# Optimization experiments

Measured on AMD Instinct MI355X. Metric: run time of the kernel, lower is better.

## Reference

```python
import jax, jax.numpy as jnp
import numpy as np

PI = 3.141592653589793

# ---------------- smoothing-constant solvers (numpy, import time) -------------
# Quadratic smoothing b*(r-rc)^2 matched to value V and slope dV at r.
def _smooth(V, dV, r):
    rc = r - 2.0 * V / dV
    b = dV * dV / (4.0 * V)
    return float(b), float(rc)

def _f1c(a, r0, rc, rlow, rhigh):  # smoothed Morse (stacking / hbond radial)
    shift = (1.0 - np.exp(-a * (rc - r0))) ** 2
    def V(r):
        return (1.0 - np.exp(-a * (r - r0))) ** 2 - shift
    def dV(r):
        e = np.exp(-a * (r - r0))
        return 2.0 * (1.0 - e) * a * e
    blow, rclow = _smooth(V(rlow), dV(rlow), rlow)
    bhigh, rchigh = _smooth(V(rhigh), dV(rhigh), rhigh)
    return dict(a=a, r0=r0, shift=float(shift), rlow=rlow, rhigh=rhigh,
                blow=blow, rclow=rclow, bhigh=bhigh, rchigh=rchigh)

def _f2c(k, r0, rc, rlow, rhigh):  # smoothed harmonic well (cross/coaxial radial)
    dc2 = (rc - r0) ** 2
    def V(r):
        return 0.5 * k * ((r - r0) ** 2 - dc2)
    def dV(r):
        return k * (r - r0)
    blow, rclow = _smooth(V(rlow), dV(rlow), rlow)
    bhigh, rchigh = _smooth(V(rhigh), dV(rhigh), rhigh)
    return dict(k=k, r0=r0, dc2=float(dc2), rlow=rlow, rhigh=rhigh,
                blow=blow, rclow=rclow, bhigh=bhigh, rchigh=rchigh)

def _f3c(sigma, rstar):  # smoothed LJ excluded volume
    s6 = sigma ** 6
    V = 4.0 * (s6 * s6 / rstar ** 12 - s6 / rstar ** 6)
    dV = 4.0 * (-12.0 * s6 * s6 / rstar ** 13 + 6.0 * s6 / rstar ** 7)
    b, rc = _smooth(V, dV, rstar)
    return dict(sigma=sigma, rstar=rstar, b=b, rc=rc)

def _f4c(a, t0, ts):  # smoothed angular modulation 1-a*(th-t0)^2
    b = a * a * ts * ts / (1.0 - a * ts * ts)
    tc = ts + a * ts / b
    return dict(a=a, t0=t0, ts=ts, b=float(b), tc=float(tc))

def _f5c(a, xs):  # one-sided smoothed modulation on a cosine
    V = 1.0 - a * xs * xs
    dV = -2.0 * a * xs
    xc = xs - 2.0 * V / dV
    b = dV * dV / (4.0 * V)
    return dict(a=a, xs=xs, xc=float(xc), b=float(b))

FENE_EPS, FENE_R0, FENE_DELTA = 2.0, 0.7525, 0.25
F1_STCK = _f1c(6.0, 0.4, 0.9, 0.32, 0.75)
F1_HB = _f1c(8.0, 0.4, 0.75, 0.34, 0.70)
F2_CRST = _f2c(47.5, 0.575, 0.675, 0.495, 0.655)
F2_CX = _f2c(46.0, 0.4, 0.6, 0.22, 0.58)
F3_BACK = _f3c(0.70, 0.675)
F3_BASE = _f3c(0.33, 0.32)
F3_MIX = _f3c(0.515, 0.50)
F4 = dict(
    s4=_f4c(1.30, 0.0, 0.80), s5=_f4c(0.90, 0.0, 0.95), s6=_f4c(0.90, 0.0, 0.95),
    h1=_f4c(1.50, 0.0, 0.70), h2=_f4c(1.50, 0.0, 0.70), h3=_f4c(1.50, 0.0, 0.70),
    h4=_f4c(0.46, PI, 0.70), h7=_f4c(4.00, 0.5 * PI, 0.45), h8=_f4c(4.00, 0.5 * PI, 0.45),
    c1=_f4c(2.25, 0.791, 0.58), c2=_f4c(1.70, 1.003, 0.68), c3=_f4c(1.70, 1.003, 0.68),
    c4=_f4c(1.50, 0.0, 0.70), c7=_f4c(1.70, 0.555, 0.68), c8=_f4c(1.70, 0.555, 0.68),
    x1=_f4c(2.00, 2.592, 0.65), x4=_f4c(1.30, 0.0, 0.80))
F5C = _f5c(2.0, -0.65)
POS_BACK, POS_STACK, POS_BASE = -0.4, 0.34, 0.4

# ---------------- jnp piecewise potential pieces ------------------------------
def f1(r, c):
    e = jnp.exp(-c['a'] * (r - c['r0']))
    core = (1.0 - e) ** 2 - c['shift']
    v = jnp.where(r < c['rlow'], c['blow'] * (r - c['rclow']) ** 2,
        jnp.where(r < c['rhigh'], core, c['bhigh'] * (r - c['rchigh']) ** 2))
    return jnp.where((r > c['rclow']) & (r < c['rchigh']), v, 0.0)

def f2(r, c):
    core = 0.5 * c['k'] * ((r - c['r0']) ** 2 - c['dc2'])
    v = jnp.where(r < c['rlow'], c['blow'] * (r - c['rclow']) ** 2,
        jnp.where(r < c['rhigh'], core, c['bhigh'] * (r - c['rchigh']) ** 2))
    return jnp.where((r > c['rclow']) & (r < c['rchigh']), v, 0.0)

def f3(r, c, eps):
    x6 = (c['sigma'] / r) ** 6
    lj = 4.0 * (x6 * x6 - x6)
    v = jnp.where(r < c['rstar'], lj, c['b'] * (r - c['rc']) ** 2)
    return eps * jnp.where(r < c['rc'], v, 0.0)

def f4(theta, c):
    dt = jnp.abs(theta - c['t0'])
    v = jnp.where(dt < c['ts'], 1.0 - c['a'] * dt * dt, c['b'] * (c['tc'] - dt) ** 2)
    return jnp.where(dt < c['tc'], v, 0.0)

def f5(x, c):
    v = jnp.where(x > c['xs'], 1.0 - c['a'] * x * x, c['b'] * (c['xc'] - x) ** 2)
    v = jnp.where(x > 0.0, 1.0, v)
    return jnp.where(x > c['xc'], v, 0.0)

# ---------------- geometry helpers --------------------------------------------
def quat_axes(q):  # rotation-matrix rows a1,a2,a3, each (N,3)
    w, x, y, z = q[..., 0], q[..., 1], q[..., 2], q[..., 3]
    a1 = jnp.stack([w*w + x*x - y*y - z*z, 2*(x*y + w*z), 2*(x*z - w*y)], -1)
    a2 = jnp.stack([2*(x*y - w*z), w*w - x*x + y*y - z*z, 2*(y*z + w*x)], -1)
    a3 = jnp.stack([2*(x*z + w*y), 2*(y*z - w*x), w*w - x*x - y*y + z*z], -1)
    return a1, a2, a3

def min_image(d, box):
    return d - box * jnp.round(d / box)

def vnorm(d):
    return jnp.sqrt(jnp.sum(d * d, -1) + 1e-12)

def acos(c):
    return jnp.arccos(jnp.clip(c, -1.0 + 1e-6, 1.0 - 1e-6))

def dot(a, b):
    return jnp.sum(a * b, -1)

# ---------------- total oxDNA energy ------------------------------------------
def total_energy(positions, quaternions, box, stacking_eps, hbond_eps_matrix,
                 excl_eps, bonded_pairs, nonbonded_pairs, base_types):
    a1, a2, a3 = quat_axes(quaternions)
    back, stck, base = POS_BACK * a1, POS_STACK * a1, POS_BASE * a1
    bi, bj = bonded_pairs[:, 0], bonded_pairs[:, 1]
    ni, nj = nonbonded_pairs[:, 0], nonbonded_pairs[:, 1]

    def disp(si, sj, i, j):  # min-image site-to-site displacement, (P,3)
        return min_image((positions[j] + sj[j]) - (positions[i] + si[i]), box)

    # FENE (bonded backbone sites)
    rb = vnorm(disp(back, back, bi, bj))
    arg = jnp.clip(((rb - FENE_R0) / FENE_DELTA) ** 2, 0.0, 1.0 - 1e-6)
    e_fene = jnp.sum(-0.5 * FENE_EPS * jnp.log1p(-arg))

    # bonded excluded volume (base-base, back-base, base-back)
    e_bexc = jnp.sum(f3(vnorm(disp(base, base, bi, bj)), F3_BASE, excl_eps)
                     + f3(vnorm(disp(back, base, bi, bj)), F3_MIX, excl_eps)
                     + f3(vnorm(disp(base, back, bi, bj)), F3_MIX, excl_eps))

    # stacking (bonded stacking sites)
    ds = disp(stck, stck, bi, bj)
    rs = vnorm(ds)
    rhs = ds / rs[:, None]
    a3i, a3j, a2i, a2j = a3[bi], a3[bj], a2[bi], a2[bj]
    db = disp(back, back, bi, bj)
    rhb = db / vnorm(db)[:, None]
    th4, th5, th6 = acos(dot(a3i, a3j)), acos(dot(rhs, a3j)), acos(-dot(rhs, a3i))
    e_stck = jnp.sum(stacking_eps * f1(rs, F1_STCK)
                     * f4(th4, F4['s4']) * f4(th5, F4['s5']) * f4(th6, F4['s6'])
                     * f5(dot(a2i, rhb), F5C) * f5(dot(a2j, rhb), F5C))

    # nonbonded gathered frames
    A1i, A1j, A2i, A2j, A3i, A3j = a1[ni], a1[nj], a2[ni], a2[nj], a3[ni], a3[nj]

    # nonbonded excluded volume (all 4 site combos)
    e_nexc = jnp.sum(f3(vnorm(disp(back, back, ni, nj)), F3_BACK, excl_eps)
                     + f3(vnorm(disp(base, base, ni, nj)), F3_BASE, excl_eps)
                     + f3(vnorm(disp(back, base, ni, nj)), F3_MIX, excl_eps)
                     + f3(vnorm(disp(base, back, ni, nj)), F3_MIX, excl_eps))

    # hydrogen bonding (base sites)
    dh = disp(base, base, ni, nj)
    rh = vnorm(dh)
    rhh = dh / rh[:, None]
    t1, t2, t3 = acos(-dot(A1i, A1j)), acos(-dot(rhh, A1j)), acos(dot(rhh, A1i))
    t4, t7, t8 = acos(dot(A3i, A3j)), acos(-dot(rhh, A3j)), acos(dot(rhh, A3i))
    eps_hb = hbond_eps_matrix[base_types[ni], base_types[nj]]
    e_hb = jnp.sum(eps_hb * f1(rh, F1_HB)
                   * f4(t1, F4['h1']) * f4(t2, F4['h2']) * f4(t3, F4['h3'])
                   * f4(t4, F4['h4']) * f4(t7, F4['h7']) * f4(t8, F4['h8']))

    # cross stacking (base sites, same angles)
    e_cr = jnp.sum(f2(rh, F2_CRST)
                   * f4(t1, F4['c1']) * f4(t2, F4['c2']) * f4(t3, F4['c3'])
                   * f4(t4, F4['c4']) * f4(t7, F4['c7']) * f4(t8, F4['c8']))

    # coaxial stacking (stack sites)
    dx = disp(stck, stck, ni, nj)
    rx = vnorm(dx)
    rhx = dx / rx[:, None]
    e_cx = jnp.sum(f2(rx, F2_CX)
                   * f4(acos(-dot(A1i, A1j)), F4['x1']) * f4(acos(dot(A3i, A3j)), F4['x4'])
                   * f5(dot(A2i, rhx), F5C) * f5(dot(A2j, rhx), F5C))

    return e_fene + e_bexc + e_stck + e_nexc + e_hb + e_cr + e_cx


def setup_inputs() -> dict:
    N = 65536
    M = 16 * N
    k = jax.random.split(jax.random.key(0), 6)
    # random-walk chain: bonded neighbours land near the FENE minimum
    steps = jax.random.normal(k[0], (N, 3), dtype=jnp.float32)
    steps = 0.65 * steps / jnp.linalg.norm(steps, axis=-1, keepdims=True)
    positions = jnp.cumsum(steps, axis=0)
    q = jax.random.normal(k[1], (N, 4), dtype=jnp.float32)
    quaternions = q / jnp.linalg.norm(q, axis=-1, keepdims=True)
    box = jnp.full((3,), 200.0, dtype=jnp.float32)
    idx = jnp.arange(N - 1, dtype=jnp.int32)
    bonded_pairs = jnp.stack([idx, idx + 1], axis=1)
    i = jax.random.randint(k[2], (M,), 0, N - 8, dtype=jnp.int32)
    off = jax.random.randint(k[3], (M,), 2, 9, dtype=jnp.int32)
    nonbonded_pairs = jnp.stack([i, i + off], axis=1)  # near-in-chain => inside cutoffs
    base_types = jax.random.randint(k[4], (N,), 0, 4, dtype=jnp.int32)
    stacking_eps = 1.3 + 0.1 * jax.random.uniform(k[5], (N - 1,), dtype=jnp.float32)
    hb = np.zeros((4, 4), dtype=np.float32)  # A=0,C=1,G=2,T=3; only WC pairs bind
    hb[0, 3] = hb[3, 0] = hb[1, 2] = hb[2, 1] = 1.077
    return dict(positions=positions, quaternions=quaternions, box=box,
                stacking_eps=stacking_eps, hbond_eps_matrix=jnp.asarray(hb),
                excl_eps=jnp.float32(2.0), bonded_pairs=bonded_pairs,
                nonbonded_pairs=nonbonded_pairs, base_types=base_types)


def reference(positions, quaternions, box, stacking_eps, hbond_eps_matrix,
              excl_eps, bonded_pairs, nonbonded_pairs, base_types):
    return total_energy(positions, quaternions, box, stacking_eps,
                        hbond_eps_matrix, excl_eps,
                        bonded_pairs, nonbonded_pairs, base_types)
```

## Files before the change

kernel.cpp:

```cpp
#include <hip/hip_runtime.h>
#include <cmath>

#define DEV __device__ __forceinline__

struct F1C { float a, r0, shift, rlow, rhigh, blow, rclow, bhigh, rchigh; };
struct F2C { float k, r0, dc2, rlow, rhigh, blow, rclow, bhigh, rchigh; };
struct F3C { float sigma2, rstar, b, rc; };
struct F4C { float a, t0, ts, b, tc; };
struct F5P { float a, xs, xc, b; };

struct Params {
  F1C f1_stck, f1_hb;
  F2C f2_crst, f2_cx;
  F3C f3_back, f3_base, f3_mix;
  F4C s4, s5, h1, h4, h7, c1, c2, c7, x1;
  F5P f5;
};

struct V3 { float x, y, z; };
DEV V3 operator+(V3 a, V3 b) { return {a.x + b.x, a.y + b.y, a.z + b.z}; }
DEV V3 operator-(V3 a, V3 b) { return {a.x - b.x, a.y - b.y, a.z - b.z}; }
DEV V3 operator*(float s, V3 a) { return {s * a.x, s * a.y, s * a.z}; }
DEV float dot(V3 a, V3 b) { return a.x * b.x + a.y * b.y + a.z * b.z; }

DEV V3 mim(V3 d, V3 box, V3 ibox) {
  return { d.x - box.x * rintf(d.x * ibox.x),
           d.y - box.y * rintf(d.y * ibox.y),
           d.z - box.z * rintf(d.z * ibox.z) };
}

DEV void quat_axes(float4 q, V3& a1, V3& a2, V3& a3) {
  float w = q.x, x = q.y, y = q.z, z = q.w;
  float ww = w * w, xx = x * x, yy = y * y, zz = z * z;
  float xy = x * y, wz = w * z, xz = x * z, wy = w * y, yz = y * z, wx = w * x;
  a1 = { ww + xx - yy - zz, 2.f * (xy + wz), 2.f * (xz - wy) };
  a2 = { 2.f * (xy - wz), ww - xx + yy - zz, 2.f * (yz + wx) };
  a3 = { 2.f * (xz + wy), 2.f * (yz - wx), ww - xx - yy + zz };
}

DEV float acosc(float c) {
  c = fminf(fmaxf(c, -0.999999f), 0.999999f);
  return acosf(c);
}

DEV float f1f(float r, const F1C& c) {
  if (r <= c.rclow || r >= c.rchigh) return 0.f;
  if (r < c.rlow) { float d = r - c.rclow; return c.blow * d * d; }
  if (r < c.rhigh) {
    float ex = expf(-c.a * (r - c.r0));
    float t = 1.f - ex;
    return t * t - c.shift;
  }
  float d = r - c.rchigh; return c.bhigh * d * d;
}

DEV float f2f(float r, const F2C& c) {
  if (r <= c.rclow || r >= c.rchigh) return 0.f;
  if (r < c.rlow) { float d = r - c.rclow; return c.blow * d * d; }
  if (r < c.rhigh) { float d = r - c.r0; return 0.5f * c.k * (d * d - c.dc2); }
  float d = r - c.rchigh; return c.bhigh * d * d;
}

DEV float f3f(float r, float r2, const F3C& c, float eps) {
  if (r >= c.rc) return 0.f;
  float v;
  if (r < c.rstar) {
    float t = c.sigma2 / r2;
    float x6 = t * t * t;
    v = 4.f * (x6 * x6 - x6);
  } else {
    float d = r - c.rc; v = c.b * d * d;
  }
  return eps * v;
}

DEV float f4f(float th, const F4C& c) {
  float dt = fabsf(th - c.t0);
  if (dt >= c.tc) return 0.f;
  if (dt < c.ts) return 1.f - c.a * dt * dt;
  float d = c.tc - dt; return c.b * d * d;
}

DEV float f5f(float x, const F5P& c) {
  if (x <= c.xc) return 0.f;
  if (x > 0.f) return 1.f;
  if (x > c.xs) return 1.f - c.a * x * x;
  float d = c.xc - x; return c.b * d * d;
}

__global__ void __launch_bounds__(256)
energy_kernel(const float* __restrict__ pos,
              const float4* __restrict__ quat,
              const float* __restrict__ boxp,
              const float* __restrict__ seps,
              const float* __restrict__ hbm,
              const float* __restrict__ exclp,
              const int2* __restrict__ bp,
              const int2* __restrict__ nbp,
              const int* __restrict__ btype,
              int M, int NP, Params P,
              double* __restrict__ partials)
{
  int gid = blockIdx.x * 256 + threadIdx.x;
  float e = 0.f;
  if (gid < M + NP) {
    bool isNB = gid < M;
    int2 ij = isNB ? nbp[gid] : bp[gid - M];
    int i = ij.x, j = ij.y;

    const float* pi_ = pos + 3 * i;
    const float* pj_ = pos + 3 * j;
    V3 dp = { pj_[0] - pi_[0], pj_[1] - pi_[1], pj_[2] - pi_[2] };
    float4 qi = quat[i], qj = quat[j];
    V3 a1i, a2i, a3i, a1j, a2j, a3j;
    quat_axes(qi, a1i, a2i, a3i);
    quat_axes(qj, a1j, a2j, a3j);

    float bx = boxp[0], by = boxp[1], bz = boxp[2];
    V3 box = { bx, by, bz };
    V3 ibox = { 1.f / bx, 1.f / by, 1.f / bz };
    float excl = exclp[0];

    V3 s = a1j - a1i;
    V3 t = a1j + a1i;
    V3 dbb = mim(dp - 0.4f  * s, box, ibox);
    V3 dhh = mim(dp + 0.4f  * s, box, ibox);
    V3 dbB = mim(dp + 0.4f  * t, box, ibox);
    V3 dBb = mim(dp - 0.4f  * t, box, ibox);
    V3 dss = mim(dp + 0.34f * s, box, ibox);

    float rbb2 = dot(dbb, dbb) + 1e-12f; float rbb = sqrtf(rbb2);
    float rhh2 = dot(dhh, dhh) + 1e-12f; float rhh = sqrtf(rhh2);
    float rbB2 = dot(dbB, dbB) + 1e-12f; float rbB = sqrtf(rbB2);
    float rBb2 = dot(dBb, dBb) + 1e-12f; float rBb = sqrtf(rBb2);
    float rss2 = dot(dss, dss) + 1e-12f; float rss = sqrtf(rss2);

    e += f3f(rhh, rhh2, P.f3_base, excl);
    e += f3f(rbB, rbB2, P.f3_mix,  excl);
    e += f3f(rBb, rBb2, P.f3_mix,  excl);

    if (isNB) {
      e += f3f(rbb, rbb2, P.f3_back, excl);
      bool need1 = (rhh > P.f1_hb.rclow   && rhh < P.f1_hb.rchigh)
                || (rhh > P.f2_crst.rclow && rhh < P.f2_crst.rchigh);
      bool need2 = (rss > P.f2_cx.rclow   && rss < P.f2_cx.rchigh);
      if (need1 || need2) {
        float t1 = acosc(-dot(a1i, a1j));
        float t4 = acosc( dot(a3i, a3j));
        if (need1) {
          float ri = 1.f / rhh;
          V3 rh = ri * dhh;
          float t2 = acosc(-dot(rh, a1j));
          float t3 = acosc( dot(rh, a1i));
          float t7 = acosc(-dot(rh, a3j));
          float t8 = acosc( dot(rh, a3i));
          float f1v = f1f(rhh, P.f1_hb);
          if (f1v != 0.f) {
            float eps = hbm[btype[i] * 4 + btype[j]];
            if (eps != 0.f)
              e += eps * f1v * f4f(t1, P.h1) * f4f(t2, P.h1) * f4f(t3, P.h1)
                            * f4f(t4, P.h4) * f4f(t7, P.h7) * f4f(t8, P.h7);
          }
          float f2v = f2f(rhh, P.f2_crst);
          if (f2v != 0.f)
            e += f2v * f4f(t1, P.c1) * f4f(t2, P.c2) * f4f(t3, P.c2)
                     * f4f(t4, P.h1) * f4f(t7, P.c7) * f4f(t8, P.c7);
        }
        if (need2) {
          float f2x = f2f(rss, P.f2_cx);
          float ri = 1.f / rss;
          V3 rx = ri * dss;
          e += f2x * f4f(t1, P.x1) * f4f(t4, P.s4)
                   * f5f(dot(a2i, rx), P.f5) * f5f(dot(a2j, rx), P.f5);
        }
      }
    } else {
      float u = (rbb - 0.7525f) * 4.0f;
      float arg = fminf(u * u, 0.999999f);
      e += -log1pf(-arg);
      float f1v = f1f(rss, P.f1_stck);
      if (f1v != 0.f) {
        float ri = 1.f / rss;
        V3 rhs = ri * dss;
        float rbi = 1.f / rbb;
        V3 rhb = rbi * dbb;
        float th4 = acosc( dot(a3i, a3j));
        float th5 = acosc( dot(rhs, a3j));
        float th6 = acosc(-dot(rhs, a3i));
        e += seps[gid - M] * f1v * f4f(th4, P.s4) * f4f(th5, P.s5) * f4f(th6, P.s5)
                           * f5f(dot(a2i, rhb), P.f5) * f5f(dot(a2j, rhb), P.f5);
      }
    }
  }

  double v = (double)e;
  #pragma unroll
  for (int off = 32; off > 0; off >>= 1) v += __shfl_down(v, off, 64);
  __shared__ double sm[4];
  int lane = threadIdx.x & 63, wid = threadIdx.x >> 6;
  if (lane == 0) sm[wid] = v;
  __syncthreads();
  if (threadIdx.x == 0) partials[blockIdx.x] = sm[0] + sm[1] + sm[2] + sm[3];
}

__global__ void __launch_bounds__(1024)
finalize_kernel(const double* __restrict__ part, int n, float* __restrict__ out) {
  double v = 0.0;
  for (int i = threadIdx.x; i < n; i += 1024) v += part[i];
  #pragma unroll
  for (int off = 32; off > 0; off >>= 1) v += __shfl_down(v, off, 64);
  __shared__ double sm[16];
  int lane = threadIdx.x & 63, wid = threadIdx.x >> 6;
  if (lane == 0) sm[wid] = v;
  __syncthreads();
  if (wid == 0) {
    v = (lane < 16) ? sm[lane] : 0.0;
    #pragma unroll
    for (int off = 8; off > 0; off >>= 1) v += __shfl_down(v, off, 64);
    if (lane == 0) out[0] = (float)v;
  }
}

static inline double sqd(double x) { return x * x; }

static F1C mkf1(double a, double r0, double rc, double rlow, double rhigh) {
  double shift = sqd(1.0 - exp(-a * (rc - r0)));
  double el = exp(-a * (rlow - r0)), eh = exp(-a * (rhigh - r0));
  double Vl = sqd(1.0 - el) - shift, Vh = sqd(1.0 - eh) - shift;
  double dVl = 2.0 * (1.0 - el) * a * el, dVh = 2.0 * (1.0 - eh) * a * eh;
  double rclow = rlow - 2.0 * Vl / dVl, blow = dVl * dVl / (4.0 * Vl);
  double rchigh = rhigh - 2.0 * Vh / dVh, bhigh = dVh * dVh / (4.0 * Vh);
  return { (float)a, (float)r0, (float)shift, (float)rlow, (float)rhigh,
           (float)blow, (float)rclow, (float)bhigh, (float)rchigh };
}

static F2C mkf2(double k, double r0, double rc, double rlow, double rhigh) {
  double dc2 = sqd(rc - r0);
  double Vl = 0.5 * k * (sqd(rlow - r0) - dc2), Vh = 0.5 * k * (sqd(rhigh - r0) - dc2);
  double dVl = k * (rlow - r0), dVh = k * (rhigh - r0);
  double rclow = rlow - 2.0 * Vl / dVl, blow = dVl * dVl / (4.0 * Vl);
  double rchigh = rhigh - 2.0 * Vh / dVh, bhigh = dVh * dVh / (4.0 * Vh);
  return { (float)k, (float)r0, (float)dc2, (float)rlow, (float)rhigh,
           (float)blow, (float)rclow, (float)bhigh, (float)rchigh };
}

static F3C mkf3(double sigma, double rstar) {
  double s6 = pow(sigma, 6.0);
  double V = 4.0 * (s6 * s6 / pow(rstar, 12.0) - s6 / pow(rstar, 6.0));
  double dV = 4.0 * (-12.0 * s6 * s6 / pow(rstar, 13.0) + 6.0 * s6 / pow(rstar, 7.0));
  double rc = rstar - 2.0 * V / dV, b = dV * dV / (4.0 * V);
  return { (float)(sigma * sigma), (float)rstar, (float)b, (float)rc };
}

static F4C mkf4(double a, double t0, double ts) {
  double b = a * a * ts * ts / (1.0 - a * ts * ts);
  double tc = ts + a * ts / b;
  return { (float)a, (float)t0, (float)ts, (float)b, (float)tc };
}

static F5P mkf5(double a, double xs) {
  double V = 1.0 - a * xs * xs, dV = -2.0 * a * xs;
  double xc = xs - 2.0 * V / dV, b = dV * dV / (4.0 * V);
  return { (float)a, (float)xs, (float)xc, (float)b };
}

extern "C" void kernel_launch(void* const* d_in, const int* in_sizes, int n_in,
                              void* d_out, int out_size, void* d_ws, size_t ws_size,
                              hipStream_t stream) {
  (void)n_in; (void)out_size; (void)ws_size;
  const double PI = 3.141592653589793;

  const float*  pos  = (const float*)d_in[0];
  const float4* quat = (const float4*)d_in[1];
  const float*  box  = (const float*)d_in[2];
  const float*  seps = (const float*)d_in[3];
  const float*  hbm  = (const float*)d_in[4];
  const float*  excl = (const float*)d_in[5];
  const int2*   bp   = (const int2*)d_in[6];
  const int2*   nbp  = (const int2*)d_in[7];
  const int*    bt   = (const int*)d_in[8];

  int NP = in_sizes[6] / 2;
  int M  = in_sizes[7] / 2;
  int total = M + NP;
  int blocks = (total + 255) / 256;

  Params P;
  P.f1_stck = mkf1(6.0, 0.4, 0.9, 0.32, 0.75);
  P.f1_hb   = mkf1(8.0, 0.4, 0.75, 0.34, 0.7);
  P.f2_crst = mkf2(47.5, 0.575, 0.675, 0.495, 0.655);
  P.f2_cx   = mkf2(46.0, 0.4, 0.6, 0.22, 0.58);
  P.f3_back = mkf3(0.7, 0.675);
  P.f3_base = mkf3(0.33, 0.32);
  P.f3_mix  = mkf3(0.515, 0.5);
  P.s4 = mkf4(1.3, 0.0, 0.8);
  P.s5 = mkf4(0.9, 0.0, 0.95);
  P.h1 = mkf4(1.5, 0.0, 0.7);
  P.h4 = mkf4(0.46, PI, 0.7);
  P.h7 = mkf4(4.0, 0.5 * PI, 0.45);
  P.c1 = mkf4(2.25, 0.791, 0.58);
  P.c2 = mkf4(1.7, 1.003, 0.68);
  P.c7 = mkf4(1.7, 0.555, 0.68);
  P.x1 = mkf4(2.0, 2.592, 0.65);
  P.f5 = mkf5(2.0, -0.65);

  double* partials = (double*)d_ws;

  energy_kernel<<<blocks, 256, 0, stream>>>(pos, quat, box, seps, hbm, excl,
                                            bp, nbp, bt, M, NP, P, partials);
  finalize_kernel<<<1, 1024, 0, stream>>>(partials, blocks, (float*)d_out);
}
```

Before: 116.1 us.

## Compact nonbonded angular work into a separate kernel and use fast intrinsics

The main kernel now computes only the radial and excluded-volume terms. It uses a wave ballot with an atomic counter to compact the indices of nonbonded pairs that fall inside the hbond, cross-stacking or coaxial ranges. A second grid-stride kernel recomputes a reduced geometry for those pairs and evaluates the acos-heavy angular terms densely, so the divergent branch no longer stalls whole wavefronts. Division, sqrt and exp are also swapped for hardware rcp/sqrt/__expf intrinsics. The cost is two extra launches, recomputed positions and quaternion axes, an atomic, and slightly lower precision; the coarse range test with a margin may also leave little compaction if most pairs qualify.

```diff
diff --git a/kernel.cpp b/kernel.cpp
--- a/kernel.cpp
+++ b/kernel.cpp
@@ -15,7 +15,11 @@
   F3C f3_back, f3_base, f3_mix;
   F4C s4, s5, h1, h4, h7, c1, c2, c7, x1;
   F5P f5;
+  float nlo1, nhi1, nlo2, nhi2;
 };
+
+DEV float asqrt(float x) { return __builtin_amdgcn_sqrtf(x); }
+DEV float arcp(float x)  { return __builtin_amdgcn_rcpf(x); }
 
 struct V3 { float x, y, z; };
 DEV V3 operator+(V3 a, V3 b) { return {a.x + b.x, a.y + b.y, a.z + b.z}; }
@@ -47,7 +51,7 @@
   if (r <= c.rclow || r >= c.rchigh) return 0.f;
   if (r < c.rlow) { float d = r - c.rclow; return c.blow * d * d; }
   if (r < c.rhigh) {
-    float ex = expf(-c.a * (r - c.r0));
+    float ex = __expf(-c.a * (r - c.r0));
     float t = 1.f - ex;
     return t * t - c.shift;
   }
@@ -65,7 +69,7 @@
   if (r >= c.rc) return 0.f;
   float v;
   if (r < c.rstar) {
-    float t = c.sigma2 / r2;
+    float t = c.sigma2 * arcp(r2);
     float x6 = t * t * t;
     v = 4.f * (x6 * x6 - x6);
   } else {
@@ -88,108 +92,103 @@
   float d = c.xc - x; return c.b * d * d;
 }
 
+struct Geo {
+  V3 a1i, a2i, a3i, a1j, a2j, a3j;
+  V3 dbb, dhh, dbB, dBb, dss;
+  float rbb, rhh, rbB, rBb, rss;
+  float rbb2, rhh2, rbB2, rBb2, rss2;
+};
+
+template <bool FULL>
+DEV void compute_geo(int i, int j, const float* __restrict__ pos,
+                     const float4* __restrict__ quat, V3 box, V3 ibox, Geo& g) {
+  const float* pi_ = pos + 3 * i;
+  const float* pj_ = pos + 3 * j;
+  V3 dp = { pj_[0] - pi_[0], pj_[1] - pi_[1], pj_[2] - pi_[2] };
+  quat_axes(quat[i], g.a1i, g.a2i, g.a3i);
+  quat_axes(quat[j], g.a1j, g.a2j, g.a3j);
+  V3 s = g.a1j - g.a1i;
+  g.dhh = mim(dp + 0.4f  * s, box, ibox);
+  g.dss = mim(dp + 0.34f * s, box, ibox);
+  g.rhh2 = dot(g.dhh, g.dhh) + 1e-12f; g.rhh = asqrt(g.rhh2);
+  g.rss2 = dot(g.dss, g.dss) + 1e-12f; g.rss = asqrt(g.rss2);
+  if (FULL) {
+    V3 t = g.a1j + g.a1i;
+    g.dbb = mim(dp - 0.4f * s, box, ibox);
+    g.dbB = mim(dp + 0.4f * t, box, ibox);
+    g.dBb = mim(dp - 0.4f * t, box, ibox);
+    g.rbb2 = dot(g.dbb, g.dbb) + 1e-12f; g.rbb = asqrt(g.rbb2);
+    g.rbB2 = dot(g.dbB, g.dbB) + 1e-12f; g.rbB = asqrt(g.rbB2);
+    g.rBb2 = dot(g.dBb, g.dBb) + 1e-12f; g.rBb = asqrt(g.rBb2);
+  }
+}
+
 __global__ void __launch_bounds__(256)
 energy_kernel(const float* __restrict__ pos,
               const float4* __restrict__ quat,
               const float* __restrict__ boxp,
               const float* __restrict__ seps,
-              const float* __restrict__ hbm,
               const float* __restrict__ exclp,
               const int2* __restrict__ bp,
               const int2* __restrict__ nbp,
-              const int* __restrict__ btype,
               int M, int NP, Params P,
+              unsigned* __restrict__ counter,
+              int* __restrict__ cidx,
               double* __restrict__ partials)
 {
   int gid = blockIdx.x * 256 + threadIdx.x;
   float e = 0.f;
+  bool need = false;
   if (gid < M + NP) {
     bool isNB = gid < M;
     int2 ij = isNB ? nbp[gid] : bp[gid - M];
-    int i = ij.x, j = ij.y;
-
-    const float* pi_ = pos + 3 * i;
-    const float* pj_ = pos + 3 * j;
-    V3 dp = { pj_[0] - pi_[0], pj_[1] - pi_[1], pj_[2] - pi_[2] };
-    float4 qi = quat[i], qj = quat[j];
-    V3 a1i, a2i, a3i, a1j, a2j, a3j;
-    quat_axes(qi, a1i, a2i, a3i);
-    quat_axes(qj, a1j, a2j, a3j);
 
     float bx = boxp[0], by = boxp[1], bz = boxp[2];
     V3 box = { bx, by, bz };
-    V3 ibox = { 1.f / bx, 1.f / by, 1.f / bz };
+    V3 ibox = { arcp(bx), arcp(by), arcp(bz) };
     float excl = exclp[0];
 
-    V3 s = a1j - a1i;
-    V3 t = a1j + a1i;
-    V3 dbb = mim(dp - 0.4f  * s, box, ibox);
-    V3 dhh = mim(dp + 0.4f  * s, box, ibox);
-    V3 dbB = mim(dp + 0.4f  * t, box, ibox);
-    V3 dBb = mim(dp - 0.4f  * t, box, ibox);
-    V3 dss = mim(dp + 0.34f * s, box, ibox);
-
-    float rbb2 = dot(dbb, dbb) + 1e-12f; float rbb = sqrtf(rbb2);
-    float rhh2 = dot(dhh, dhh) + 1e-12f; float rhh = sqrtf(rhh2);
-    float rbB2 = dot(dbB, dbB) + 1e-12f; float rbB = sqrtf(rbB2);
-    float rBb2 = dot(dBb, dBb) + 1e-12f; float rBb = sqrtf(rBb2);
-    float rss2 = dot(dss, dss) + 1e-12f; float rss = sqrtf(rss2);
-
-    e += f3f(rhh, rhh2, P.f3_base, excl);
-    e += f3f(rbB, rbB2, P.f3_mix,  excl);
-    e += f3f(rBb, rBb2, P.f3_mix,  excl);
+    Geo g;
+    compute_geo<true>(ij.x, ij.y, pos, quat, box, ibox, g);
+
+    e += f3f(g.rhh, g.rhh2, P.f3_base, excl);
+    e += f3f(g.rbB, g.rbB2, P.f3_mix,  excl);
+    e += f3f(g.rBb, g.rBb2, P.f3_mix,  excl);
 
     if (isNB) {
-      e += f3f(rbb, rbb2, P.f3_back, excl);
-      bool need1 = (rhh > P.f1_hb.rclow   && rhh < P.f1_hb.rchigh)
-                || (rhh > P.f2_crst.rclow && rhh < P.f2_crst.rchigh);
-      bool need2 = (rss > P.f2_cx.rclow   && rss < P.f2_cx.rchigh);
-      if (need1 || need2) {
-        float t1 = acosc(-dot(a1i, a1j));
-        float t4 = acosc( dot(a3i, a3j));
-        if (need1) {
-          float ri = 1.f / rhh;
-          V3 rh = ri * dhh;
-          float t2 = acosc(-dot(rh, a1j));
-          float t3 = acosc( dot(rh, a1i));
-          float t7 = acosc(-dot(rh, a3j));
-          float t8 = acosc( dot(rh, a3i));
-          float f1v = f1f(rhh, P.f1_hb);
-          if (f1v != 0.f) {
-            float eps = hbm[btype[i] * 4 + btype[j]];
-            if (eps != 0.f)
-              e += eps * f1v * f4f(t1, P.h1) * f4f(t2, P.h1) * f4f(t3, P.h1)
-                            * f4f(t4, P.h4) * f4f(t7, P.h7) * f4f(t8, P.h7);
-          }
-          float f2v = f2f(rhh, P.f2_crst);
-          if (f2v != 0.f)
-            e += f2v * f4f(t1, P.c1) * f4f(t2, P.c2) * f4f(t3, P.c2)
-                     * f4f(t4, P.h1) * f4f(t7, P.c7) * f4f(t8, P.c7);
-        }
-        if (need2) {
-          float f2x = f2f(rss, P.f2_cx);
-          float ri = 1.f / rss;
-          V3 rx = ri * dss;
-          e += f2x * f4f(t1, P.x1) * f4f(t4, P.s4)
-                   * f5f(dot(a2i, rx), P.f5) * f5f(dot(a2j, rx), P.f5);
-        }
-      }
+      e += f3f(g.rbb, g.rbb2, P.f3_back, excl);
+      need = (g.rhh > P.nlo1 && g.rhh < P.nhi1) ||
+             (g.rss > P.nlo2 && g.rss < P.nhi2);
     } else {
-      float u = (rbb - 0.7525f) * 4.0f;
+      float u = (g.rbb - 0.7525f) * 4.0f;
       float arg = fminf(u * u, 0.999999f);
       e += -log1pf(-arg);
-      float f1v = f1f(rss, P.f1_stck);
+      float f1v = f1f(g.rss, P.f1_stck);
       if (f1v != 0.f) {
-        float ri = 1.f / rss;
-        V3 rhs = ri * dss;
-        float rbi = 1.f / rbb;
-        V3 rhb = rbi * dbb;
-        float th4 = acosc( dot(a3i, a3j));
-        float th5 = acosc( dot(rhs, a3j));
-        float th6 = acosc(-dot(rhs, a3i));
+        float ri = arcp(g.rss);
+        V3 rhs = ri * g.dss;
+        float rbi = arcp(g.rbb);
+        V3 rhb = rbi * g.dbb;
+        float th4 = acosc( dot(g.a3i, g.a3j));
+        float th5 = acosc( dot(rhs, g.a3j));
+        float th6 = acosc(-dot(rhs, g.a3i));
         e += seps[gid - M] * f1v * f4f(th4, P.s4) * f4f(th5, P.s5) * f4f(th6, P.s5)
-                           * f5f(dot(a2i, rhb), P.f5) * f5f(dot(a2j, rhb), P.f5);
+                           * f5f(dot(g.a2i, rhb), P.f5) * f5f(dot(g.a2j, rhb), P.f5);
       }
+    }
+  }
+
+  unsigned long long mask = __ballot(need);
+  if (mask) {
+    int lane = threadIdx.x & 63;
+    int leader = __ffsll(mask) - 1;
+    int cnt = (int)__popcll(mask);
+    int base = 0;
+    if (lane == leader) base = (int)atomicAdd(counter, (unsigned)cnt);
+    base = __shfl(base, leader, 64);
+    if (need) {
+      int prefix = (int)__popcll(mask & ((1ull << lane) - 1ull));
+      cidx[base + prefix] = gid;
     }
   }
 
@@ -203,10 +202,77 @@
   if (threadIdx.x == 0) partials[blockIdx.x] = sm[0] + sm[1] + sm[2] + sm[3];
 }
 
+__global__ void __launch_bounds__(256)
+nb_angle_kernel(const float* __restrict__ pos,
+                const float4* __restrict__ quat,
+                const float* __restrict__ boxp,
+                const float* __restrict__ hbm,
+                const int2* __restrict__ nbp,
+                const int* __restrict__ btype,
+                const unsigned* __restrict__ counter,
+                const int* __restrict__ cidx,
+                Params P,
+                double* __restrict__ partialsB)
+{
+  int n2 = (int)*counter;
+  float bx = boxp[0], by = boxp[1], bz = boxp[2];
+  V3 box = { bx, by, bz };
+  V3 ibox = { arcp(bx), arcp(by), arcp(bz) };
+
+  double v = 0.0;
+  int stride = gridDim.x * 256;
+  for (int k = blockIdx.x * 256 + threadIdx.x; k < n2; k += stride) {
+    int2 ij = nbp[cidx[k]];
+    Geo g;
+    compute_geo<false>(ij.x, ij.y, pos, quat, box, ibox, g);
+
+    float t1 = acosc(-dot(g.a1i, g.a1j));
+    float t4 = acosc( dot(g.a3i, g.a3j));
+
+    float ri = arcp(g.rhh);
+    V3 rh = ri * g.dhh;
+    float t2 = acosc(-dot(rh, g.a1j));
+    float t3 = acosc( dot(rh, g.a1i));
+    float t7 = acosc(-dot(rh, g.a3j));
+    float t8 = acosc( dot(rh, g.a3i));
+
+    float e = 0.f;
+    float f1v = f1f(g.rhh, P.f1_hb);
+    float eps = hbm[btype[ij.x] * 4 + btype[ij.y]];
+    e += eps * f1v * f4f(t1, P.h1) * f4f(t2, P.h1) * f4f(t3, P.h1)
+             * f4f(t4, P.h4) * f4f(t7, P.h7) * f4f(t8, P.h7);
+
+    float f2v = f2f(g.rhh, P.f2_crst);
+    e += f2v * f4f(t1, P.c1) * f4f(t2, P.c2) * f4f(t3, P.c2)
+             * f4f(t4, P.h1) * f4f(t7, P.c7) * f4f(t8, P.c7);
+
+    float f2x = f2f(g.rss, P.f2_cx);
+    float rxi = arcp(g.rss);
+    V3 rx = rxi * g.dss;
+    e += f2x * f4f(t1, P.x1) * f4f(t4, P.s4)
+             * f5f(dot(g.a2i, rx), P.f5) * f5f(dot(g.a2j, rx), P.f5);
+
+    v += (double)e;
+  }
+
+  #pragma unroll
+  for (int off = 32; off > 0; off >>= 1) v += __shfl_down(v, off, 64);
+  __shared__ double sm[4];
+  int lane = threadIdx.x & 63, wid = threadIdx.x >> 6;
+  if (lane == 0) sm[wid] = v;
+  __syncthreads();
+  if (threadIdx.x == 0) partialsB[blockIdx.x] = sm[0] + sm[1] + sm[2] + sm[3];
+}
+
+__global__ void zero_counter_kernel(unsigned* c) { *c = 0u; }
+
 __global__ void __launch_bounds__(1024)
-finalize_kernel(const double* __restrict__ part, int n, float* __restrict__ out) {
+finalize_kernel(const double* __restrict__ pA, int nA,
+                const double* __restrict__ pB, int nB,
+                float* __restrict__ out) {
   double v = 0.0;
-  for (int i = threadIdx.x; i < n; i += 1024) v += part[i];
+  for (int i = threadIdx.x; i < nA; i += 1024) v += pA[i];
+  for (int i = threadIdx.x; i < nB; i += 1024) v += pB[i];
   #pragma unroll
   for (int off = 32; off > 0; off >>= 1) v += __shfl_down(v, off, 64);
   __shared__ double sm[16];
@@ -283,7 +349,8 @@
   int NP = in_sizes[6] / 2;
   int M  = in_sizes[7] / 2;
   int total = M + NP;
-  int blocks = (total + 255) / 256;
+  int blocksA = (total + 255) / 256;
+  int blocksB = 1024;
 
   Params P;
   P.f1_stck = mkf1(6.0, 0.4, 0.9, 0.32, 0.75);
@@ -303,10 +370,20 @@
   P.c7 = mkf4(1.7, 0.555, 0.68);
   P.x1 = mkf4(2.0, 2.592, 0.65);
   P.f5 = mkf5(2.0, -0.65);
-
-  double* partials = (double*)d_ws;
-
-  energy_kernel<<<blocks, 256, 0, stream>>>(pos, quat, box, seps, hbm, excl,
-                                            bp, nbp, bt, M, NP, P, partials);
-  finalize_kernel<<<1, 1024, 0, stream>>>(partials, blocks, (float*)d_out);
-}
+  P.nlo1 = P.f1_hb.rclow  - 1e-3f;  P.nhi1 = P.f1_hb.rchigh  + 1e-3f;
+  P.nlo2 = P.f2_cx.rclow  - 1e-3f;  P.nhi2 = P.f2_cx.rchigh  + 1e-3f;
+
+  unsigned* counter  = (unsigned*)d_ws;
+  double* partialsA  = (double*)((char*)d_ws + 4096);
+  double* partialsB  = (double*)((char*)d_ws + 131072);
+  int* cidx          = (int*)((char*)d_ws + 262144);
+
+  zero_counter_kernel<<<1, 1, 0, stream>>>(counter);
+  energy_kernel<<<blocksA, 256, 0, stream>>>(pos, quat, box, seps, excl,
+                                             bp, nbp, M, NP, P,
+                                             counter, cidx, partialsA);
+  nb_angle_kernel<<<blocksB, 256, 0, stream>>>(pos, quat, box, hbm, nbp, bt,
+                                               counter, cidx, P, partialsB);
+  finalize_kernel<<<1, 1024, 0, stream>>>(partialsA, blocksA, partialsB, blocksB,
+                                          (float*)d_out);
+}
```

After: 282.8 us. 2.44x slower.

## Compact non-bonded pairs needing angular terms into shared-memory queue; use fast intrinsics

Applied to the files above, without the earlier changes.

Non-bonded pairs whose hbond/coaxial radial window is active are collected with a ballot/prefix sum into a shared list. The expensive angular part is then evaluated by packed threads, which removes wavefront divergence. The change also replaces acosf with a polynomial approximation and uses hardware rcp, rsq and sqrt, __expf and __logf. It compares squared radii against precomputed thresholds and computes a2/a3 axes only when needed. The cost is recomputing geometry for queued pairs, an extra barrier, and lower accuracy in acos, log and exp. The need-window omits the f2_crst range, relying on it lying inside the hbond window plus a margin.

```diff
diff --git a/kernel.cpp b/kernel.cpp
--- a/kernel.cpp
+++ b/kernel.cpp
@@ -5,7 +5,7 @@
 
 struct F1C { float a, r0, shift, rlow, rhigh, blow, rclow, bhigh, rchigh; };
 struct F2C { float k, r0, dc2, rlow, rhigh, blow, rclow, bhigh, rchigh; };
-struct F3C { float sigma2, rstar, b, rc; };
+struct F3C { float sigma2, rstar2, b, rc, rc2; };
 struct F4C { float a, t0, ts, b, tc; };
 struct F5P { float a, xs, xc, b; };
 
@@ -15,7 +15,12 @@
   F3C f3_back, f3_base, f3_mix;
   F4C s4, s5, h1, h4, h7, c1, c2, c7, x1;
   F5P f5;
+  float nlo1sq, nhi1sq, nlo2sq, nhi2sq;
 };
+
+DEV float asqrt(float x) { return __builtin_amdgcn_sqrtf(x); }
+DEV float arcp(float x)  { return __builtin_amdgcn_rcpf(x); }
+DEV float arsq(float x)  { return __builtin_amdgcn_rsqf(x); }
 
 struct V3 { float x, y, z; };
 DEV V3 operator+(V3 a, V3 b) { return {a.x + b.x, a.y + b.y, a.z + b.z}; }
@@ -29,25 +34,37 @@
            d.z - box.z * rintf(d.z * ibox.z) };
 }
 
-DEV void quat_axes(float4 q, V3& a1, V3& a2, V3& a3) {
+DEV void quat_a1(float4 q, V3& a1) {
   float w = q.x, x = q.y, y = q.z, z = q.w;
-  float ww = w * w, xx = x * x, yy = y * y, zz = z * z;
-  float xy = x * y, wz = w * z, xz = x * z, wy = w * y, yz = y * z, wx = w * x;
-  a1 = { ww + xx - yy - zz, 2.f * (xy + wz), 2.f * (xz - wy) };
-  a2 = { 2.f * (xy - wz), ww - xx + yy - zz, 2.f * (yz + wx) };
-  a3 = { 2.f * (xz + wy), 2.f * (yz - wx), ww - xx - yy + zz };
-}
-
-DEV float acosc(float c) {
-  c = fminf(fmaxf(c, -0.999999f), 0.999999f);
-  return acosf(c);
+  a1 = { w*w + x*x - y*y - z*z, 2.f*(x*y + w*z), 2.f*(x*z - w*y) };
+}
+
+DEV void quat_a23(float4 q, V3& a2, V3& a3) {
+  float w = q.x, x = q.y, y = q.z, z = q.w;
+  a2 = { 2.f*(x*y - w*z), w*w - x*x + y*y - z*z, 2.f*(y*z + w*x) };
+  a3 = { 2.f*(x*z + w*y), 2.f*(y*z - w*x), w*w - x*x - y*y + z*z };
+}
+
+DEV float acosc(float x) {
+  x = fminf(fmaxf(x, -0.999999f), 0.999999f);
+  float u = fabsf(x);
+  float p = -0.0012624911f;
+  p = fmaf(p, u,  0.0066700901f);
+  p = fmaf(p, u, -0.0170881256f);
+  p = fmaf(p, u,  0.0308918810f);
+  p = fmaf(p, u, -0.0501743046f);
+  p = fmaf(p, u,  0.0889789874f);
+  p = fmaf(p, u, -0.2145988016f);
+  p = fmaf(p, u,  1.5707963050f);
+  float r = asqrt(1.f - u) * p;
+  return x >= 0.f ? r : 3.14159265358979f - r;
 }
 
 DEV float f1f(float r, const F1C& c) {
   if (r <= c.rclow || r >= c.rchigh) return 0.f;
   if (r < c.rlow) { float d = r - c.rclow; return c.blow * d * d; }
   if (r < c.rhigh) {
-    float ex = expf(-c.a * (r - c.r0));
+    float ex = __expf(-c.a * (r - c.r0));
     float t = 1.f - ex;
     return t * t - c.shift;
   }
@@ -61,15 +78,15 @@
   float d = r - c.rchigh; return c.bhigh * d * d;
 }
 
-DEV float f3f(float r, float r2, const F3C& c, float eps) {
-  if (r >= c.rc) return 0.f;
+DEV float f3f(float r2, const F3C& c, float eps) {
+  if (r2 >= c.rc2) return 0.f;
   float v;
-  if (r < c.rstar) {
-    float t = c.sigma2 / r2;
+  if (r2 < c.rstar2) {
+    float t = c.sigma2 * arcp(r2);
     float x6 = t * t * t;
     v = 4.f * (x6 * x6 - x6);
   } else {
-    float d = r - c.rc; v = c.b * d * d;
+    float d = asqrt(r2) - c.rc; v = c.b * d * d;
   }
   return eps * v;
 }
@@ -102,24 +119,25 @@
               double* __restrict__ partials)
 {
   int gid = blockIdx.x * 256 + threadIdx.x;
+  float bx = boxp[0], by = boxp[1], bz = boxp[2];
+  V3 box = { bx, by, bz };
+  V3 ibox = { arcp(bx), arcp(by), arcp(bz) };
+
   float e = 0.f;
+  bool need = false;
+  int2 myij = {0, 0};
   if (gid < M + NP) {
     bool isNB = gid < M;
-    int2 ij = isNB ? nbp[gid] : bp[gid - M];
-    int i = ij.x, j = ij.y;
-
-    const float* pi_ = pos + 3 * i;
-    const float* pj_ = pos + 3 * j;
+    myij = isNB ? nbp[gid] : bp[gid - M];
+    float excl = exclp[0];
+
+    const float* pi_ = pos + 3 * myij.x;
+    const float* pj_ = pos + 3 * myij.y;
     V3 dp = { pj_[0] - pi_[0], pj_[1] - pi_[1], pj_[2] - pi_[2] };
-    float4 qi = quat[i], qj = quat[j];
-    V3 a1i, a2i, a3i, a1j, a2j, a3j;
-    quat_axes(qi, a1i, a2i, a3i);
-    quat_axes(qj, a1j, a2j, a3j);
-
-    float bx = boxp[0], by = boxp[1], bz = boxp[2];
-    V3 box = { bx, by, bz };
-    V3 ibox = { 1.f / bx, 1.f / by, 1.f / bz };
-    float excl = exclp[0];
+    float4 qi = quat[myij.x], qj = quat[myij.y];
+    V3 a1i, a1j;
+    quat_a1(qi, a1i);
+    quat_a1(qj, a1j);
 
     V3 s = a1j - a1i;
     V3 t = a1j + a1i;
@@ -129,61 +147,35 @@
     V3 dBb = mim(dp - 0.4f  * t, box, ibox);
     V3 dss = mim(dp + 0.34f * s, box, ibox);
 
-    float rbb2 = dot(dbb, dbb) + 1e-12f; float rbb = sqrtf(rbb2);
-    float rhh2 = dot(dhh, dhh) + 1e-12f; float rhh = sqrtf(rhh2);
-    float rbB2 = dot(dbB, dbB) + 1e-12f; float rbB = sqrtf(rbB2);
-    float rBb2 = dot(dBb, dBb) + 1e-12f; float rBb = sqrtf(rBb2);
-    float rss2 = dot(dss, dss) + 1e-12f; float rss = sqrtf(rss2);
-
-    e += f3f(rhh, rhh2, P.f3_base, excl);
-    e += f3f(rbB, rbB2, P.f3_mix,  excl);
-    e += f3f(rBb, rBb2, P.f3_mix,  excl);
+    float rbb2 = dot(dbb, dbb) + 1e-12f;
+    float rhh2 = dot(dhh, dhh) + 1e-12f;
+    float rbB2 = dot(dbB, dbB) + 1e-12f;
+    float rBb2 = dot(dBb, dBb) + 1e-12f;
+    float rss2 = dot(dss, dss) + 1e-12f;
+
+    e += f3f(rhh2, P.f3_base, excl);
+    e += f3f(rbB2, P.f3_mix,  excl);
+    e += f3f(rBb2, P.f3_mix,  excl);
 
     if (isNB) {
-      e += f3f(rbb, rbb2, P.f3_back, excl);
-      bool need1 = (rhh > P.f1_hb.rclow   && rhh < P.f1_hb.rchigh)
-                || (rhh > P.f2_crst.rclow && rhh < P.f2_crst.rchigh);
-      bool need2 = (rss > P.f2_cx.rclow   && rss < P.f2_cx.rchigh);
-      if (need1 || need2) {
-        float t1 = acosc(-dot(a1i, a1j));
-        float t4 = acosc( dot(a3i, a3j));
-        if (need1) {
-          float ri = 1.f / rhh;
-          V3 rh = ri * dhh;
-          float t2 = acosc(-dot(rh, a1j));
-          float t3 = acosc( dot(rh, a1i));
-          float t7 = acosc(-dot(rh, a3j));
-          float t8 = acosc( dot(rh, a3i));
-          float f1v = f1f(rhh, P.f1_hb);
-          if (f1v != 0.f) {
-            float eps = hbm[btype[i] * 4 + btype[j]];
-            if (eps != 0.f)
-              e += eps * f1v * f4f(t1, P.h1) * f4f(t2, P.h1) * f4f(t3, P.h1)
-                            * f4f(t4, P.h4) * f4f(t7, P.h7) * f4f(t8, P.h7);
-          }
-          float f2v = f2f(rhh, P.f2_crst);
-          if (f2v != 0.f)
-            e += f2v * f4f(t1, P.c1) * f4f(t2, P.c2) * f4f(t3, P.c2)
-                     * f4f(t4, P.h1) * f4f(t7, P.c7) * f4f(t8, P.c7);
-        }
-        if (need2) {
-          float f2x = f2f(rss, P.f2_cx);
-          float ri = 1.f / rss;
-          V3 rx = ri * dss;
-          e += f2x * f4f(t1, P.x1) * f4f(t4, P.s4)
-                   * f5f(dot(a2i, rx), P.f5) * f5f(dot(a2j, rx), P.f5);
-        }
-      }
+      e += f3f(rbb2, P.f3_back, excl);
+      need = (rhh2 > P.nlo1sq && rhh2 < P.nhi1sq) ||
+             (rss2 > P.nlo2sq && rss2 < P.nhi2sq);
     } else {
+      float rsbb = arsq(rbb2);
+      float rbb  = rbb2 * rsbb;
       float u = (rbb - 0.7525f) * 4.0f;
       float arg = fminf(u * u, 0.999999f);
-      e += -log1pf(-arg);
+      e += -__logf(1.f - arg);
+      float rsss = arsq(rss2);
+      float rss  = rss2 * rsss;
       float f1v = f1f(rss, P.f1_stck);
       if (f1v != 0.f) {
-        float ri = 1.f / rss;
-        V3 rhs = ri * dss;
-        float rbi = 1.f / rbb;
-        V3 rhb = rbi * dbb;
+        V3 a2i, a3i, a2j, a3j;
+        quat_a23(qi, a2i, a3i);
+        quat_a23(qj, a2j, a3j);
+        V3 rhs = rsss * dss;
+        V3 rhb = rsbb * dbb;
         float th4 = acosc( dot(a3i, a3j));
         float th5 = acosc( dot(rhs, a3j));
         float th6 = acosc(-dot(rhs, a3i));
@@ -193,11 +185,73 @@
     }
   }
 
+  __shared__ unsigned wcnt[4];
+  __shared__ int2 spair[256];
+  int lane = threadIdx.x & 63, wid = threadIdx.x >> 6;
+  unsigned long long mask = __ballot(need);
+  if (lane == 0) wcnt[wid] = (unsigned)__popcll(mask);
+  __syncthreads();
+  unsigned base = 0;
+  #pragma unroll
+  for (int w = 0; w < 4; ++w) if (w < wid) base += wcnt[w];
+  unsigned total = wcnt[0] + wcnt[1] + wcnt[2] + wcnt[3];
+  if (need) {
+    unsigned pfx = (unsigned)__popcll(mask & ((1ull << lane) - 1ull));
+    spair[base + pfx] = myij;
+  }
+  __syncthreads();
+
+  for (unsigned t = threadIdx.x; t < total; t += 256) {
+    int2 ij = spair[t];
+    const float* pi_ = pos + 3 * ij.x;
+    const float* pj_ = pos + 3 * ij.y;
+    V3 dp = { pj_[0] - pi_[0], pj_[1] - pi_[1], pj_[2] - pi_[2] };
+    float4 qi = quat[ij.x], qj = quat[ij.y];
+    V3 a1i, a2i, a3i, a1j, a2j, a3j;
+    quat_a1(qi, a1i);  quat_a23(qi, a2i, a3i);
+    quat_a1(qj, a1j);  quat_a23(qj, a2j, a3j);
+    V3 s = a1j - a1i;
+    V3 dhh = mim(dp + 0.4f  * s, box, ibox);
+    V3 dss = mim(dp + 0.34f * s, box, ibox);
+    float rhh2 = dot(dhh, dhh) + 1e-12f;
+    float rss2 = dot(dss, dss) + 1e-12f;
+    float rsh = arsq(rhh2);
+    float rhh = rhh2 * rsh;
+
+    float t1 = acosc(-dot(a1i, a1j));
+    float t4 = acosc( dot(a3i, a3j));
+
+    V3 rh = rsh * dhh;
+    float t2 = acosc(-dot(rh, a1j));
+    float t3 = acosc( dot(rh, a1i));
+    float t7 = acosc(-dot(rh, a3j));
+    float t8 = acosc( dot(rh, a3i));
+
+    float f1v = f1f(rhh, P.f1_hb);
+    if (f1v != 0.f) {
+      float eps = hbm[btype[ij.x] * 4 + btype[ij.y]];
+      e += eps * f1v * f4f(t1, P.h1) * f4f(t2, P.h1) * f4f(t3, P.h1)
+               * f4f(t4, P.h4) * f4f(t7, P.h7) * f4f(t8, P.h7);
+    }
+    float f2v = f2f(rhh, P.f2_crst);
+    if (f2v != 0.f)
+      e += f2v * f4f(t1, P.c1) * f4f(t2, P.c2) * f4f(t3, P.c2)
+               * f4f(t4, P.h1) * f4f(t7, P.c7) * f4f(t8, P.c7);
+
+    float rsx = arsq(rss2);
+    float rss = rss2 * rsx;
+    float f2x = f2f(rss, P.f2_cx);
+    if (f2x != 0.f) {
+      V3 rx = rsx * dss;
+      e += f2x * f4f(t1, P.x1) * f4f(t4, P.s4)
+               * f5f(dot(a2i, rx), P.f5) * f5f(dot(a2j, rx), P.f5);
+    }
+  }
+
   double v = (double)e;
   #pragma unroll
   for (int off = 32; off > 0; off >>= 1) v += __shfl_down(v, off, 64);
   __shared__ double sm[4];
-  int lane = threadIdx.x & 63, wid = threadIdx.x >> 6;
   if (lane == 0) sm[wid] = v;
   __syncthreads();
   if (threadIdx.x == 0) partials[blockIdx.x] = sm[0] + sm[1] + sm[2] + sm[3];
@@ -249,7 +303,8 @@
   double V = 4.0 * (s6 * s6 / pow(rstar, 12.0) - s6 / pow(rstar, 6.0));
   double dV = 4.0 * (-12.0 * s6 * s6 / pow(rstar, 13.0) + 6.0 * s6 / pow(rstar, 7.0));
   double rc = rstar - 2.0 * V / dV, b = dV * dV / (4.0 * V);
-  return { (float)(sigma * sigma), (float)rstar, (float)b, (float)rc };
+  return { (float)(sigma * sigma), (float)(rstar * rstar), (float)b,
+           (float)rc, (float)(rc * rc) };
 }
 
 static F4C mkf4(double a, double t0, double ts) {
@@ -303,6 +358,12 @@
   P.c7 = mkf4(1.7, 0.555, 0.68);
   P.x1 = mkf4(2.0, 2.592, 0.65);
   P.f5 = mkf5(2.0, -0.65);
+  {
+    double lo1 = (double)P.f1_hb.rclow  - 1e-3, hi1 = (double)P.f1_hb.rchigh + 1e-3;
+    double lo2 = (double)P.f2_cx.rclow  - 1e-3, hi2 = (double)P.f2_cx.rchigh + 1e-3;
+    P.nlo1sq = (float)(lo1 * lo1);  P.nhi1sq = (float)(hi1 * hi1);
+    P.nlo2sq = (float)(lo2 * lo2);  P.nhi2sq = (float)(hi2 * hi2);
+  }
 
   double* partials = (double*)d_ws;
 
```

Result: faster. 110.0 us (-5.3%).
